# Performance work log

Hardware: AMD Instinct MI355X
Metric: run time of the kernel (lower is better)

The kernel has to match this reference:

```python
import jax, jax.numpy as jnp
import numpy as np

H = 1.0  # primo_h
N_GRID = 768


def _grid_mesh(n):
    ii, jj = np.meshgrid(np.arange(n - 1), np.arange(n - 1), indexing='ij')
    v00 = (ii * n + jj).ravel(); v10 = ((ii + 1) * n + jj).ravel()
    v01 = (ii * n + jj + 1).ravel(); v11 = ((ii + 1) * n + jj + 1).ravel()
    tri1 = np.stack([v00, v10, v01], 1); tri2 = np.stack([v10, v11, v01], 1)
    return np.concatenate([tri1, tri2], 0).astype(np.int32)  # [F,3]


def _face_adjacency(faces):
    # faces: [F,3] -> edges [E,2] (sorted vertex pairs), face_ids [E,2]
    F = faces.shape[0]
    fe = np.stack([faces[:, [0, 1]], faces[:, [1, 2]], faces[:, [2, 0]]], 1).reshape(-1, 2)
    fe = np.sort(fe, axis=1)
    fid = np.repeat(np.arange(F, dtype=np.int32), 3)
    order = np.lexsort((fe[:, 1], fe[:, 0]))
    fs, fi = fe[order], fid[order]
    same = np.all(fs[:-1] == fs[1:], axis=1)
    k = np.nonzero(same)[0]
    edges = fs[k].astype(np.int32)
    face_ids = np.stack([fi[k], fi[k + 1]], 1).astype(np.int32)
    return edges, face_ids


def setup_inputs() -> dict:
    key = jax.random.key(0)
    k1, k2, k3 = jax.random.split(key, 3)
    faces_np = _grid_mesh(N_GRID)                      # [F,3]
    edges_np, face_ids_np = _face_adjacency(faces_np)  # [E,2],[E,2]
    F = faces_np.shape[0]
    V = N_GRID * N_GRID
    return {
        'transformed_prism': jax.random.normal(k1, (F, 3, 3), dtype=jnp.float32),
        'rotations': jax.random.normal(k2, (F, 3, 3), dtype=jnp.float32),
        'verts': jax.random.normal(k3, (1, V, 3), dtype=jnp.float32),
        'faces': jnp.asarray(faces_np.T),       # [3,F], matches torch forward arg
        'edges': jnp.asarray(edges_np),
        'face_ids': jnp.asarray(face_ids_np),
    }


def _verts_id_face(Ft, E, Q):
    # Ft: [F,3] faces; E: [e,2] edge vertex ids; Q: [e,2] adjacent face ids
    fa, fb = Ft[Q[:, 0]], Ft[Q[:, 1]]  # [e,3]

    def find(fv, tgt):
        return jnp.where(fv[:, 0] == tgt, 0,
               jnp.where(fv[:, 1] == tgt, 1,
               jnp.where(fv[:, 2] == tgt, 2, -1)))

    return jnp.stack([find(fa, E[:, 0]), find(fa, E[:, 1]),
                      find(fb, E[:, 0]), find(fb, E[:, 1])], axis=1)  # [e,4]


def reference(transformed_prism, rotations, verts, faces, edges, face_ids):
    tp = transformed_prism
    bs = verts.shape[0]
    v = verts.reshape(-1, 3)
    Ft = faces.T  # [F,3]

    # per-face normals (vectorized version of the original per-face loop)
    e1 = tp[:, 0] - tp[:, 1]
    e2 = tp[:, 0] - tp[:, 2]
    nrm = jnp.cross(e1, e2)
    normals = nrm / jnp.linalg.norm(nrm, axis=-1, keepdims=True)  # [F,3]

    # face areas
    p1, p2, p3 = v[Ft[:, 0]], v[Ft[:, 1]], v[Ft[:, 2]]
    face_areas = 0.5 * jnp.linalg.norm(jnp.cross(p2 - p1, p3 - p1), axis=1)

    # faithful to original: normals indexed by edge VERTEX ids
    n1, n2 = normals[edges[:, 0]], normals[edges[:, 1]]
    fid1, fid2 = face_ids[:, 0], face_ids[:, 1]
    r1, r2 = rotations[fid1], rotations[fid2]

    ftv = _verts_id_face(Ft, edges, face_ids)  # [e,4]
    v1_p1, v2_p1 = tp[fid1, ftv[:, 0]], tp[fid1, ftv[:, 1]]
    v1_p2, v2_p2 = tp[fid2, ftv[:, 2]], tp[fid2, ftv[:, 3]]

    p1n1 = jnp.einsum('ec,ecd->ed', n1, r1)
    p1n2 = jnp.einsum('ec,ecd->ed', n2, r1)
    p2n1 = jnp.einsum('ec,ecd->ed', n1, r2)
    p2n2 = jnp.einsum('ec,ecd->ed', n2, r2)

    A = jnp.stack([v1_p1 + p1n1 * H, v2_p1 + p1n2 * H,
                   v1_p1 - p1n1 * H, v2_p1 - p1n2 * H], axis=1)  # [e,4,3]
    B = jnp.stack([v1_p2 + p2n1 * H, v2_p2 + p2n2 * H,
                   v1_p2 - p2n1 * H, v2_p2 - p2n2 * H], axis=1)
    D = A - B

    # coeff[p,q] = 2^{-|i_p-i_q|-|j_p-j_q|}, (i,j) over {0,1}^2
    idx = jnp.array([[0, 0], [0, 1], [1, 0], [1, 1]], dtype=jnp.float32)
    coeff = 2.0 ** (-jnp.abs(idx[:, None] - idx[None, :]).sum(-1))  # [4,4]
    pair = jnp.einsum('epc,eqc->epq', D, D)
    energy = (pair * coeff).sum((1, 2)) / 9.0  # [e]

    weight = jnp.sum((v[edges[:, 0]] - v[edges[:, 1]]) ** 2, axis=1) \
             / (face_areas[fid1] + face_areas[fid2])
    return (energy * weight).sum() / bs
```

## Files before the change

### kernel.cpp

```cpp
#include <hip/hip_runtime.h>


#define BI 8
#define BJ 32
#define T2ROW 288
#define VROW  100
#define NSTRIDE 99
#define T2_CH 648
#define V_CH  250
#define NORM_CNT 297
#define HALO_CNT 192

struct __attribute__((aligned(4))) F4s { float a, b, c, d; };
struct F3 { float x, y, z; };
struct R9 { float v[9]; };

__device__ __forceinline__ R9 load9(const float* __restrict__ p) {
    R9 r;
    F4s u0 = *(const F4s*)p;
    F4s u1 = *(const F4s*)(p + 4);
    r.v[0] = u0.a; r.v[1] = u0.b; r.v[2] = u0.c; r.v[3] = u0.d;
    r.v[4] = u1.a; r.v[5] = u1.b; r.v[6] = u1.c; r.v[7] = u1.d;
    r.v[8] = p[8];
    return r;
}

__device__ __forceinline__ int imin(int a, int b) { return a < b ? a : b; }
__device__ __forceinline__ int imax(int a, int b) { return a > b ? a : b; }

__device__ __forceinline__ void gload_lds16(const float* gp, float* lp) {
    __builtin_amdgcn_global_load_lds(
        (const __attribute__((address_space(1))) void*)gp,
        (__attribute__((address_space(3))) void*)lp, 16, 0, 0);
}

__device__ __forceinline__ F3 normal_of(const R9& r) {
    float e1x = r.v[0] - r.v[3], e1y = r.v[1] - r.v[4], e1z = r.v[2] - r.v[5];
    float e2x = r.v[0] - r.v[6], e2y = r.v[1] - r.v[7], e2z = r.v[2] - r.v[8];
    float nx = e1y * e2z - e1z * e2y;
    float ny = e1z * e2x - e1x * e2z;
    float nz = e1x * e2y - e1y * e2x;
    float inv = 1.0f / sqrtf(nx * nx + ny * ny + nz * nz);
    F3 o; o.x = nx * inv; o.y = ny * inv; o.z = nz * inv; return o;
}

__device__ __forceinline__ float tri_area_p(const float* p, const float* q,
                                            const float* r) {
    float ax = q[0] - p[0], ay = q[1] - p[1], az = q[2] - p[2];
    float bx = r[0] - p[0], by = r[1] - p[1], bz = r[2] - p[2];
    float cx = ay * bz - az * by, cy = az * bx - ax * bz, cz = ax * by - ay * bx;
    return 0.5f * sqrtf(cx * cx + cy * cy + cz * cz);
}

__device__ __forceinline__ float edge_ew(const float* u1, const float* u2,
                                         const float* w1, const float* w2,
                                         const float* rA, const float* rB,
                                         const F3& n1, const F3& n2,
                                         const float* pa, const float* pb,
                                         float asum) {
    float ux = u1[0] - u2[0], uy = u1[1] - u2[1], uz = u1[2] - u2[2];
    float wx = w1[0] - w2[0], wy = w1[1] - w2[1], wz = w1[2] - w2[2];

    float d0 = rA[0] - rB[0], d1 = rA[1] - rB[1], d2 = rA[2] - rB[2];
    float d3 = rA[3] - rB[3], d4 = rA[4] - rB[4], d5 = rA[5] - rB[5];
    float d6 = rA[6] - rB[6], d7 = rA[7] - rB[7], d8 = rA[8] - rB[8];

    float ax = n1.x * d0 + n1.y * d3 + n1.z * d6;
    float ay = n1.x * d1 + n1.y * d4 + n1.z * d7;
    float az = n1.x * d2 + n1.y * d5 + n1.z * d8;
    float bx = n2.x * d0 + n2.y * d3 + n2.z * d6;
    float by = n2.x * d1 + n2.y * d4 + n2.z * d7;
    float bz = n2.x * d2 + n2.y * d5 + n2.z * d8;

    float uu = ux * ux + uy * uy + uz * uz;
    float ww = wx * wx + wy * wy + wz * wz;
    float uw = ux * wx + uy * wy + uz * wz;
    float aa = ax * ax + ay * ay + az * az;
    float bb = bx * bx + by * by + bz * bz;
    float ab = ax * bx + ay * by + az * bz;
    float energy = (3.0f * (uu + ww + uw) + (aa + bb + ab)) * (1.0f / 9.0f);

    float dx = pa[0] - pb[0], dy = pa[1] - pb[1], dz = pa[2] - pb[2];
    return energy * (dx * dx + dy * dy + dz * dz) / asum;
}

__global__ __launch_bounds__(256) void fused_kernel(
        const float* __restrict__ tp,
        const float* __restrict__ rot,
        const float* __restrict__ verts,
        double* __restrict__ partials,
        int n) {
    const int m = n - 1;
    const int Q = m * m;
    const int F = 2 * Q;
    const int V = n * n;
    const int tid = threadIdx.x;
    const int i0 = blockIdx.y * BI;
    const int j0 = blockIdx.x * BJ;
    const int w = tid >> 5;
    const int l = tid & 31;
    const int i = i0 + w;
    const int j = j0 + l;
    const int wv = tid >> 6;
    const int lane = tid & 63;

    __shared__ __attribute__((aligned(16))) float sT2m[9 * T2ROW];
    __shared__ __attribute__((aligned(16))) float sR2m[9 * T2ROW];
    __shared__ __attribute__((aligned(16))) float sVm[10 * VROW];
    __shared__ float sN[9 * NSTRIDE];
    __shared__ float sT2h[9 * 12];
    __shared__ float sR2h[9 * 12];
    __shared__ float sVh[10 * 4];
    __shared__ double sred[4];

    int f1 = imin(i, m - 1) * m + imin(j, m - 1);
    R9 t1 = load9(tp  + (size_t)9 * f1);
    R9 r1 = load9(rot + (size_t)9 * f1);

#pragma unroll
    for (int it = 0; it < 7; ++it) {
        int ws = it * 4 + wv;
        if (ws < 22) {
            int a = ws >= 11;
            int wl = a ? ws - 11 : ws;
            int chunk = wl * 64 + lane;
            if (chunk < T2_CH) {
                int r = chunk / 72, c = chunk - r * 72;
                int gi = imin(i0 - 1 + r, m - 1);
                int g = 9 * (Q + gi * m + j0) + 4 * c;
                g = imin(g, 9 * F - 4);
                gload_lds16((a ? rot : tp) + g,
                            (a ? sR2m : sT2m) + chunk * 4);
            }
        } else if (ws < 26) {
            int chunk = (ws - 22) * 64 + lane;
            if (chunk < V_CH) {
                int r = chunk / 25, c = chunk - r * 25;
                int vr = imax(imin(i0 - 1 + r, n - 1), 0);
                int g = 3 * (vr * n + j0) + 4 * c;
                g = imin(g, 3 * V - 4);
                gload_lds16(verts + g, sVm + chunk * 4);
            }
        }
    }

    float hval = 0.0f;
    float* hdst = nullptr;
    if (tid < HALO_CNT) {
        if (tid < 162) {
            int a = tid >= 81;
            int t = a ? tid - 81 : tid;
            int r = t / 9, k = t - 9 * r;
            int gi = imin(i0 - 1 + r, m - 1);
            int face = Q + gi * m + (j0 - 1);
            hval = (a ? rot : tp)[9 * face + k];
            hdst = (a ? sR2h : sT2h) + r * 12 + k;
        } else {
            int t = tid - 162;
            int r = t / 3, k = t - 3 * r;
            int vr = imax(imin(i0 - 1 + r, n - 1), 0);
            int g = imax(3 * (vr * n + (j0 - 1)) + k, 0);
            hval = verts[g];
            hdst = sVh + r * 4 + k;
        }
    }

    R9 nraw[2];
    int nofs[2];
#pragma unroll
    for (int it = 0; it < 2; ++it) {
        int s = tid + 256 * it;
        bool act = s < NORM_CNT;
        int sc = act ? s : 0;
        int r = sc / 33, c = sc - 33 * r;
        int gi = imin(i0 + r, n - 1);
        int gj = imin(j0 + c, n - 1);
        nraw[it] = load9(tp + (size_t)9 * (gi * n + gj));
        nofs[it] = act ? (r * NSTRIDE + 3 * c) : -1;
    }

    if (hdst) *hdst = hval;
#pragma unroll
    for (int it = 0; it < 2; ++it) {
        if (nofs[it] >= 0) {
            F3 nm = normal_of(nraw[it]);
            sN[nofs[it]] = nm.x; sN[nofs[it] + 1] = nm.y; sN[nofs[it] + 2] = nm.z;
        }
    }

    __syncthreads();

    double term = 0.0;
    if (i < m && j < m) {
        const float* t2c = sT2m + (w + 1) * T2ROW + 9 * l;
        const float* r2c = sR2m + (w + 1) * T2ROW + 9 * l;
        const float* th  = sT2m + w * T2ROW + 9 * l;
        const float* rh  = sR2m + w * T2ROW + 9 * l;
        const float* tv  = l ? sT2m + (w + 1) * T2ROW + 9 * (l - 1)
                             : sT2h + (w + 1) * 12;
        const float* rv  = l ? sR2m + (w + 1) * T2ROW + 9 * (l - 1)
                             : sR2h + (w + 1) * 12;

        const float* p00 = sVm + (w + 1) * VROW + 3 * l;
        const float* p01 = p00 + 3;
        const float* p10 = sVm + (w + 2) * VROW + 3 * l;
        const float* p11 = p10 + 3;
        const float* pup = sVm + w * VROW + 3 * (l + 1);
        const float* plf = l ? sVm + (w + 2) * VROW + 3 * (l - 1)
                             : sVh + (w + 2) * 4;

        const float* na = sN + w * NSTRIDE + 3 * l;
        const float* nb = na + 3;
        const float* nc = sN + (w + 1) * NSTRIDE + 3 * l;
        F3 nA = { na[0], na[1], na[2] };
        F3 nB = { nb[0], nb[1], nb[2] };
        F3 nC = { nc[0], nc[1], nc[2] };

        float a1   = tri_area_p(p00, p10, p01);
        float a2c  = tri_area_p(p10, p11, p01);
        float a2up = tri_area_p(p00, p01, pup);
        float a2lf = tri_area_p(plf, p10, p00);

        float sum = edge_ew(t1.v + 6, t2c + 6, t1.v + 3, t2c + 0, r1.v, r2c,
                            nB, nC, p01, p10, a1 + a2c);
        float eh = edge_ew(t1.v + 0, th + 0, t1.v + 6, th + 3, r1.v, rh,
                           nA, nB, p00, p01, a1 + a2up);
        float ev = edge_ew(t1.v + 0, tv + 6, t1.v + 3, tv + 3, r1.v, rv,
                           nA, nC, p00, p10, a1 + a2lf);
        sum += (i > 0 ? eh : 0.0f);
        sum += (j > 0 ? ev : 0.0f);
        term = (double)sum;
    }

#pragma unroll
    for (int off = 32; off > 0; off >>= 1) term += __shfl_down(term, off, 64);
    if (lane == 0) sred[wv] = term;
    __syncthreads();
    if (tid == 0)
        partials[blockIdx.y * gridDim.x + blockIdx.x] =
            sred[0] + sred[1] + sred[2] + sred[3];
}

__global__ __launch_bounds__(256) void finalize_kernel(
        const double* __restrict__ partials, int P, float* __restrict__ out) {
    double s = 0.0;
    for (int i = threadIdx.x; i < P; i += 256) s += partials[i];
#pragma unroll
    for (int off = 32; off > 0; off >>= 1) s += __shfl_down(s, off, 64);
    __shared__ double sred[4];
    int lane = threadIdx.x & 63, wid = threadIdx.x >> 6;
    if (lane == 0) sred[wid] = s;
    __syncthreads();
    if (threadIdx.x == 0) out[0] = (float)(sred[0] + sred[1] + sred[2] + sred[3]);
}

extern "C" void kernel_launch(void* const* d_in, const int* in_sizes, int n_in,
                              void* d_out, int out_size, void* d_ws, size_t ws_size,
                              hipStream_t stream) {
    const float* tp    = (const float*)d_in[0];
    const float* rot   = (const float*)d_in[1];
    const float* verts = (const float*)d_in[2];

    int V = in_sizes[2] / 3;
    int n = (int)(sqrtf((float)V) + 0.5f);
    int m = n - 1;

    double* partials = (double*)d_ws;
    float*  out      = (float*)d_out;

    dim3 grid((m + BJ - 1) / BJ, (m + BI - 1) / BI);
    int P = grid.x * grid.y;
    fused_kernel<<<grid, 256, 0, stream>>>(tp, rot, verts, partials, n);
    finalize_kernel<<<1, 256, 0, stream>>>(partials, P, out);
}
```

Before: 145.5 us.

## Shrink tile to 8x8 single-wavefront blocks and fold halo into main loads

Changes the tile from 8x32 faces with 256 threads to 8x8 faces with a single 64-lane wavefront per block. The left halo column of second-triangle data is now loaded as part of the main tile, so the separate halo buffers and left-edge special cases for tp/rot go away. The block reduction no longer needs shared memory or a barrier, since one wave writes its partial directly. The cost is a larger halo fraction, with more redundant global loads per face, four times as many blocks, and a larger partials array for the finalize kernel to sum serially.

```diff
diff --git a/kernel.cpp b/kernel.cpp
--- a/kernel.cpp
+++ b/kernel.cpp
@@ -2,14 +2,13 @@
 
 
 #define BI 8
-#define BJ 32
-#define T2ROW 288
-#define VROW  100
-#define NSTRIDE 99
-#define T2_CH 648
-#define V_CH  250
-#define NORM_CNT 297
-#define HALO_CNT 192
+#define BJ 8
+#define T2ROW 84
+#define VROW  28
+#define NSTRIDE 28
+#define T2_CH 189
+#define V_CH  70
+#define NORM_CNT 81
 
 struct __attribute__((aligned(4))) F4s { float a, b, c, d; };
 struct F3 { float x, y, z; };
@@ -84,7 +83,7 @@
     return energy * (dx * dx + dy * dy + dz * dz) / asum;
 }
 
-__global__ __launch_bounds__(256) void fused_kernel(
+__global__ __launch_bounds__(64) void fused_kernel(
         const float* __restrict__ tp,
         const float* __restrict__ rot,
         const float* __restrict__ verts,
@@ -94,85 +93,67 @@
     const int Q = m * m;
     const int F = 2 * Q;
     const int V = n * n;
-    const int tid = threadIdx.x;
+    const int lane = threadIdx.x;
     const int i0 = blockIdx.y * BI;
     const int j0 = blockIdx.x * BJ;
-    const int w = tid >> 5;
-    const int l = tid & 31;
+    const int w = lane >> 3;
+    const int l = lane & 7;
     const int i = i0 + w;
     const int j = j0 + l;
-    const int wv = tid >> 6;
-    const int lane = tid & 63;
-
-    __shared__ __attribute__((aligned(16))) float sT2m[9 * T2ROW];
-    __shared__ __attribute__((aligned(16))) float sR2m[9 * T2ROW];
-    __shared__ __attribute__((aligned(16))) float sVm[10 * VROW];
+
+    __shared__ __attribute__((aligned(16))) float sT2[9 * T2ROW];
+    __shared__ __attribute__((aligned(16))) float sR2[9 * T2ROW];
+    __shared__ __attribute__((aligned(16))) float sV[10 * VROW];
+    __shared__ float sVh[10 * 4];
     __shared__ float sN[9 * NSTRIDE];
-    __shared__ float sT2h[9 * 12];
-    __shared__ float sR2h[9 * 12];
-    __shared__ float sVh[10 * 4];
-    __shared__ double sred[4];
 
     int f1 = imin(i, m - 1) * m + imin(j, m - 1);
     R9 t1 = load9(tp  + (size_t)9 * f1);
     R9 r1 = load9(rot + (size_t)9 * f1);
 
 #pragma unroll
-    for (int it = 0; it < 7; ++it) {
-        int ws = it * 4 + wv;
-        if (ws < 22) {
-            int a = ws >= 11;
-            int wl = a ? ws - 11 : ws;
-            int chunk = wl * 64 + lane;
-            if (chunk < T2_CH) {
-                int r = chunk / 72, c = chunk - r * 72;
+    for (int it = 0; it < 8; ++it) {
+        if (it < 6) {
+            int a = it >= 3;
+            int ch = (a ? it - 3 : it) * 64 + lane;
+            if (ch < T2_CH) {
+                int r = ch / 21, c = ch - 21 * r;
                 int gi = imin(i0 - 1 + r, m - 1);
-                int g = 9 * (Q + gi * m + j0) + 4 * c;
+                int g = 9 * (Q + gi * m + (j0 - 1)) + 4 * c;
                 g = imin(g, 9 * F - 4);
                 gload_lds16((a ? rot : tp) + g,
-                            (a ? sR2m : sT2m) + chunk * 4);
+                            (a ? sR2 : sT2) + ch * 4);
             }
-        } else if (ws < 26) {
-            int chunk = (ws - 22) * 64 + lane;
-            if (chunk < V_CH) {
-                int r = chunk / 25, c = chunk - r * 25;
+        } else {
+            int ch = (it - 6) * 64 + lane;
+            if (ch < V_CH) {
+                int r = ch / 7, c = ch - 7 * r;
                 int vr = imax(imin(i0 - 1 + r, n - 1), 0);
                 int g = 3 * (vr * n + j0) + 4 * c;
                 g = imin(g, 3 * V - 4);
-                gload_lds16(verts + g, sVm + chunk * 4);
+                gload_lds16(verts + g, sV + ch * 4);
             }
         }
     }
 
     float hval = 0.0f;
     float* hdst = nullptr;
-    if (tid < HALO_CNT) {
-        if (tid < 162) {
-            int a = tid >= 81;
-            int t = a ? tid - 81 : tid;
-            int r = t / 9, k = t - 9 * r;
-            int gi = imin(i0 - 1 + r, m - 1);
-            int face = Q + gi * m + (j0 - 1);
-            hval = (a ? rot : tp)[9 * face + k];
-            hdst = (a ? sR2h : sT2h) + r * 12 + k;
-        } else {
-            int t = tid - 162;
-            int r = t / 3, k = t - 3 * r;
-            int vr = imax(imin(i0 - 1 + r, n - 1), 0);
-            int g = imax(3 * (vr * n + (j0 - 1)) + k, 0);
-            hval = verts[g];
-            hdst = sVh + r * 4 + k;
-        }
+    if (lane < 30) {
+        int r = lane / 3, k = lane - 3 * r;
+        int vr = imax(imin(i0 - 1 + r, n - 1), 0);
+        int g = imax(3 * (vr * n + (j0 - 1)) + k, 0);
+        hval = verts[g];
+        hdst = sVh + r * 4 + k;
     }
 
     R9 nraw[2];
     int nofs[2];
 #pragma unroll
     for (int it = 0; it < 2; ++it) {
-        int s = tid + 256 * it;
+        int s = lane + 64 * it;
         bool act = s < NORM_CNT;
         int sc = act ? s : 0;
-        int r = sc / 33, c = sc - 33 * r;
+        int r = sc / 9, c = sc - 9 * r;
         int gi = imin(i0 + r, n - 1);
         int gj = imin(j0 + c, n - 1);
         nraw[it] = load9(tp + (size_t)9 * (gi * n + gj));
@@ -192,21 +173,19 @@
 
     double term = 0.0;
     if (i < m && j < m) {
-        const float* t2c = sT2m + (w + 1) * T2ROW + 9 * l;
-        const float* r2c = sR2m + (w + 1) * T2ROW + 9 * l;
-        const float* th  = sT2m + w * T2ROW + 9 * l;
-        const float* rh  = sR2m + w * T2ROW + 9 * l;
-        const float* tv  = l ? sT2m + (w + 1) * T2ROW + 9 * (l - 1)
-                             : sT2h + (w + 1) * 12;
-        const float* rv  = l ? sR2m + (w + 1) * T2ROW + 9 * (l - 1)
-                             : sR2h + (w + 1) * 12;
-
-        const float* p00 = sVm + (w + 1) * VROW + 3 * l;
+        const float* t2c = sT2 + (w + 1) * T2ROW + 9 * (l + 1);
+        const float* r2c = sR2 + (w + 1) * T2ROW + 9 * (l + 1);
+        const float* th  = sT2 + w * T2ROW + 9 * (l + 1);
+        const float* rh  = sR2 + w * T2ROW + 9 * (l + 1);
+        const float* tv  = sT2 + (w + 1) * T2ROW + 9 * l;
+        const float* rv  = sR2 + (w + 1) * T2ROW + 9 * l;
+
+        const float* p00 = sV + (w + 1) * VROW + 3 * l;
         const float* p01 = p00 + 3;
-        const float* p10 = sVm + (w + 2) * VROW + 3 * l;
+        const float* p10 = sV + (w + 2) * VROW + 3 * l;
         const float* p11 = p10 + 3;
-        const float* pup = sVm + w * VROW + 3 * (l + 1);
-        const float* plf = l ? sVm + (w + 2) * VROW + 3 * (l - 1)
+        const float* pup = sV + w * VROW + 3 * (l + 1);
+        const float* plf = l ? sV + (w + 2) * VROW + 3 * (l - 1)
                              : sVh + (w + 2) * 4;
 
         const float* na = sN + w * NSTRIDE + 3 * l;
@@ -234,11 +213,8 @@
 
 #pragma unroll
     for (int off = 32; off > 0; off >>= 1) term += __shfl_down(term, off, 64);
-    if (lane == 0) sred[wv] = term;
-    __syncthreads();
-    if (tid == 0)
-        partials[blockIdx.y * gridDim.x + blockIdx.x] =
-            sred[0] + sred[1] + sred[2] + sred[3];
+    if (lane == 0)
+        partials[blockIdx.y * gridDim.x + blockIdx.x] = term;
 }
 
 __global__ __launch_bounds__(256) void finalize_kernel(
@@ -270,6 +246,6 @@
 
     dim3 grid((m + BJ - 1) / BJ, (m + BI - 1) / BI);
     int P = grid.x * grid.y;
-    fused_kernel<<<grid, 256, 0, stream>>>(tp, rot, verts, partials, n);
+    fused_kernel<<<grid, 64, 0, stream>>>(tp, rot, verts, partials, n);
     finalize_kernel<<<1, 256, 0, stream>>>(partials, P, out);
 }
```

Result: slower. 159.5 us (+9.6%).

## Make blocks persistent over several tiles with double-buffered LDS prefetch

Applied to the files above, without the earlier changes.

Each block now handles three consecutive 8x32 tiles and double-buffers the shared-memory staging, so the next tile's async global-to-LDS loads and register loads are issued before the current tile is computed. The separate left-halo face loads are folded into a wider main DMA row of 75 chunks. This aims to hide load latency behind compute and cut per-block startup cost. In exchange, LDS use roughly doubles, which may lower occupancy, and there are fewer blocks across the GPU.

```diff
diff --git a/kernel.cpp b/kernel.cpp
--- a/kernel.cpp
+++ b/kernel.cpp
@@ -1,19 +1,18 @@
 #include <hip/hip_runtime.h>
 
 
-#define BI 8
-#define BJ 32
-#define T2ROW 288
-#define VROW  100
-#define NSTRIDE 99
-#define T2_CH 648
-#define V_CH  250
-#define NORM_CNT 297
-#define HALO_CNT 192
+#define FST 300
+#define F_SLOTS 675
+#define VST 100
+#define V_SLOTS 250
+#define NST 99
+#define NCNT 297
+#define TPB 3
 
 struct __attribute__((aligned(4))) F4s { float a, b, c, d; };
 struct F3 { float x, y, z; };
 struct R9 { float v[9]; };
+struct TileRegs { R9 t1, r1, nraw0, nraw1; float hval; };
 
 __device__ __forceinline__ R9 load9(const float* __restrict__ p) {
     R9 r;
@@ -95,123 +94,122 @@
     const int F = 2 * Q;
     const int V = n * n;
     const int tid = threadIdx.x;
-    const int i0 = blockIdx.y * BI;
-    const int j0 = blockIdx.x * BJ;
+    const int wv = tid >> 6;
+    const int lane = tid & 63;
     const int w = tid >> 5;
     const int l = tid & 31;
-    const int i = i0 + w;
-    const int j = j0 + l;
-    const int wv = tid >> 6;
-    const int lane = tid & 63;
-
-    __shared__ __attribute__((aligned(16))) float sT2m[9 * T2ROW];
-    __shared__ __attribute__((aligned(16))) float sR2m[9 * T2ROW];
-    __shared__ __attribute__((aligned(16))) float sVm[10 * VROW];
-    __shared__ float sN[9 * NSTRIDE];
-    __shared__ float sT2h[9 * 12];
-    __shared__ float sR2h[9 * 12];
-    __shared__ float sVh[10 * 4];
+
+    const int nTj = (m + 31) / 32;
+    const int nTi = (m + 7) / 8;
+    const int nT = nTi * nTj;
+
+    __shared__ __attribute__((aligned(16))) float sT2[2][9 * FST];
+    __shared__ __attribute__((aligned(16))) float sR2[2][9 * FST];
+    __shared__ __attribute__((aligned(16))) float sV[2][10 * VST];
+    __shared__ float sN[2][9 * NST];
+    __shared__ float sVh[2][10 * 4];
     __shared__ double sred[4];
 
-    int f1 = imin(i, m - 1) * m + imin(j, m - 1);
-    R9 t1 = load9(tp  + (size_t)9 * f1);
-    R9 r1 = load9(rot + (size_t)9 * f1);
-
+    auto stage_dma = [&](int p, int i0, int j0) {
 #pragma unroll
-    for (int it = 0; it < 7; ++it) {
-        int ws = it * 4 + wv;
-        if (ws < 22) {
-            int a = ws >= 11;
-            int wl = a ? ws - 11 : ws;
-            int chunk = wl * 64 + lane;
-            if (chunk < T2_CH) {
-                int r = chunk / 72, c = chunk - r * 72;
-                int gi = imin(i0 - 1 + r, m - 1);
-                int g = 9 * (Q + gi * m + j0) + 4 * c;
-                g = imin(g, 9 * F - 4);
-                gload_lds16((a ? rot : tp) + g,
-                            (a ? sR2m : sT2m) + chunk * 4);
+        for (int it = 0; it < 7; ++it) {
+            int ws = it * 4 + wv;
+            if (ws < 22) {
+                int a = ws >= 11;
+                int wl = a ? ws - 11 : ws;
+                int ch = wl * 64 + lane;
+                if (ch < F_SLOTS) {
+                    int r = ch / 75, c = ch - 75 * r;
+                    int gi = imin(i0 - 1 + r, m - 1);
+                    int g = 9 * (Q + gi * m + (j0 - 1)) + 4 * c;
+                    g = imin(g, 9 * F - 4);
+                    gload_lds16((a ? rot : tp) + g,
+                                (a ? sR2[p] : sT2[p]) + ch * 4);
+                }
+            } else if (ws < 26) {
+                int ch = (ws - 22) * 64 + lane;
+                if (ch < V_SLOTS) {
+                    int r = ch / 25, c = ch - 25 * r;
+                    int vr = imax(imin(i0 - 1 + r, n - 1), 0);
+                    int g = 3 * (vr * n + j0) + 4 * c;
+                    g = imin(g, 3 * V - 4);
+                    gload_lds16(verts + g, sV[p] + ch * 4);
+                }
             }
-        } else if (ws < 26) {
-            int chunk = (ws - 22) * 64 + lane;
-            if (chunk < V_CH) {
-                int r = chunk / 25, c = chunk - r * 25;
-                int vr = imax(imin(i0 - 1 + r, n - 1), 0);
-                int g = 3 * (vr * n + j0) + 4 * c;
-                g = imin(g, 3 * V - 4);
-                gload_lds16(verts + g, sVm + chunk * 4);
-            }
-        }
-    }
-
-    float hval = 0.0f;
-    float* hdst = nullptr;
-    if (tid < HALO_CNT) {
-        if (tid < 162) {
-            int a = tid >= 81;
-            int t = a ? tid - 81 : tid;
-            int r = t / 9, k = t - 9 * r;
-            int gi = imin(i0 - 1 + r, m - 1);
-            int face = Q + gi * m + (j0 - 1);
-            hval = (a ? rot : tp)[9 * face + k];
-            hdst = (a ? sR2h : sT2h) + r * 12 + k;
-        } else {
-            int t = tid - 162;
-            int r = t / 3, k = t - 3 * r;
+        }
+    };
+
+    auto stage_regs = [&](TileRegs& tr, int i0, int j0) {
+        int i = i0 + w, j = j0 + l;
+        int f1 = imin(i, m - 1) * m + imin(j, m - 1);
+        tr.t1 = load9(tp  + (size_t)9 * f1);
+        tr.r1 = load9(rot + (size_t)9 * f1);
+        {
+            int s = tid;
+            int r = s / 33, c = s - 33 * r;
+            int gi = imin(i0 + r, n - 1), gj = imin(j0 + c, n - 1);
+            tr.nraw0 = load9(tp + (size_t)9 * (size_t)(gi * n + gj));
+        }
+        {
+            int s = tid + 256;
+            int sc = (s < NCNT) ? s : 0;
+            int r = sc / 33, c = sc - 33 * r;
+            int gi = imin(i0 + r, n - 1), gj = imin(j0 + c, n - 1);
+            tr.nraw1 = load9(tp + (size_t)9 * (size_t)(gi * n + gj));
+        }
+        tr.hval = 0.0f;
+        if (tid < 30) {
+            int r = tid / 3, k = tid - 3 * r;
             int vr = imax(imin(i0 - 1 + r, n - 1), 0);
-            int g = imax(3 * (vr * n + (j0 - 1)) + k, 0);
-            hval = verts[g];
-            hdst = sVh + r * 4 + k;
-        }
-    }
-
-    R9 nraw[2];
-    int nofs[2];
-#pragma unroll
-    for (int it = 0; it < 2; ++it) {
-        int s = tid + 256 * it;
-        bool act = s < NORM_CNT;
-        int sc = act ? s : 0;
-        int r = sc / 33, c = sc - 33 * r;
-        int gi = imin(i0 + r, n - 1);
-        int gj = imin(j0 + c, n - 1);
-        nraw[it] = load9(tp + (size_t)9 * (gi * n + gj));
-        nofs[it] = act ? (r * NSTRIDE + 3 * c) : -1;
-    }
-
-    if (hdst) *hdst = hval;
-#pragma unroll
-    for (int it = 0; it < 2; ++it) {
-        if (nofs[it] >= 0) {
-            F3 nm = normal_of(nraw[it]);
-            sN[nofs[it]] = nm.x; sN[nofs[it] + 1] = nm.y; sN[nofs[it] + 2] = nm.z;
-        }
-    }
-
-    __syncthreads();
-
-    double term = 0.0;
-    if (i < m && j < m) {
-        const float* t2c = sT2m + (w + 1) * T2ROW + 9 * l;
-        const float* r2c = sR2m + (w + 1) * T2ROW + 9 * l;
-        const float* th  = sT2m + w * T2ROW + 9 * l;
-        const float* rh  = sR2m + w * T2ROW + 9 * l;
-        const float* tv  = l ? sT2m + (w + 1) * T2ROW + 9 * (l - 1)
-                             : sT2h + (w + 1) * 12;
-        const float* rv  = l ? sR2m + (w + 1) * T2ROW + 9 * (l - 1)
-                             : sR2h + (w + 1) * 12;
-
-        const float* p00 = sVm + (w + 1) * VROW + 3 * l;
+            tr.hval = verts[imax(3 * (vr * n + (j0 - 1)) + k, 0)];
+        }
+    };
+
+    auto write_regs = [&](int p, TileRegs& tr) {
+        {
+            int s = tid;
+            int r = s / 33, c = s - 33 * r;
+            F3 nm = normal_of(tr.nraw0);
+            int o = r * NST + 3 * c;
+            sN[p][o] = nm.x; sN[p][o + 1] = nm.y; sN[p][o + 2] = nm.z;
+        }
+        if (tid + 256 < NCNT) {
+            int s = tid + 256;
+            int r = s / 33, c = s - 33 * r;
+            F3 nm = normal_of(tr.nraw1);
+            int o = r * NST + 3 * c;
+            sN[p][o] = nm.x; sN[p][o + 1] = nm.y; sN[p][o + 2] = nm.z;
+        }
+        if (tid < 30) {
+            int r = tid / 3, k = tid - 3 * r;
+            sVh[p][r * 4 + k] = tr.hval;
+        }
+    };
+
+    auto compute_tile = [&](int p, int i0, int j0, const TileRegs& tr) -> double {
+        int i = i0 + w, j = j0 + l;
+        if (i >= m || j >= m) return 0.0;
+        const float* fT = sT2[p];
+        const float* fR = sR2[p];
+        const float* t2c = fT + (w + 1) * FST + 9 * (l + 1);
+        const float* r2c = fR + (w + 1) * FST + 9 * (l + 1);
+        const float* th  = fT + w * FST + 9 * (l + 1);
+        const float* rh  = fR + w * FST + 9 * (l + 1);
+        const float* tv  = fT + (w + 1) * FST + 9 * l;
+        const float* rv  = fR + (w + 1) * FST + 9 * l;
+
+        const float* vb = sV[p];
+        const float* p00 = vb + (w + 1) * VST + 3 * l;
         const float* p01 = p00 + 3;
-        const float* p10 = sVm + (w + 2) * VROW + 3 * l;
+        const float* p10 = vb + (w + 2) * VST + 3 * l;
         const float* p11 = p10 + 3;
-        const float* pup = sVm + w * VROW + 3 * (l + 1);
-        const float* plf = l ? sVm + (w + 2) * VROW + 3 * (l - 1)
-                             : sVh + (w + 2) * 4;
-
-        const float* na = sN + w * NSTRIDE + 3 * l;
+        const float* pup = vb + w * VST + 3 * (l + 1);
+        const float* plf = l ? vb + (w + 2) * VST + 3 * (l - 1)
+                             : sVh[p] + (w + 2) * 4;
+
+        const float* na = sN[p] + w * NST + 3 * l;
         const float* nb = na + 3;
-        const float* nc = sN + (w + 1) * NSTRIDE + 3 * l;
+        const float* nc = sN[p] + (w + 1) * NST + 3 * l;
         F3 nA = { na[0], na[1], na[2] };
         F3 nB = { nb[0], nb[1], nb[2] };
         F3 nC = { nc[0], nc[1], nc[2] };
@@ -221,24 +219,69 @@
         float a2up = tri_area_p(p00, p01, pup);
         float a2lf = tri_area_p(plf, p10, p00);
 
-        float sum = edge_ew(t1.v + 6, t2c + 6, t1.v + 3, t2c + 0, r1.v, r2c,
-                            nB, nC, p01, p10, a1 + a2c);
-        float eh = edge_ew(t1.v + 0, th + 0, t1.v + 6, th + 3, r1.v, rh,
-                           nA, nB, p00, p01, a1 + a2up);
-        float ev = edge_ew(t1.v + 0, tv + 6, t1.v + 3, tv + 3, r1.v, rv,
-                           nA, nC, p00, p10, a1 + a2lf);
+        float sum = edge_ew(tr.t1.v + 6, t2c + 6, tr.t1.v + 3, t2c + 0,
+                            tr.r1.v, r2c, nB, nC, p01, p10, a1 + a2c);
+        float eh = edge_ew(tr.t1.v + 0, th + 0, tr.t1.v + 6, th + 3,
+                           tr.r1.v, rh, nA, nB, p00, p01, a1 + a2up);
+        float ev = edge_ew(tr.t1.v + 0, tv + 6, tr.t1.v + 3, tv + 3,
+                           tr.r1.v, rv, nA, nC, p00, p10, a1 + a2lf);
         sum += (i > 0 ? eh : 0.0f);
         sum += (j > 0 ? ev : 0.0f);
-        term = (double)sum;
+        return (double)sum;
+    };
+
+    const int tau0 = blockIdx.x * TPB;
+    TileRegs regA, regB;
+
+    {
+        int tau = tau0;
+        if (tau < nT) {
+            int ti = tau / nTj, tj = tau - ti * nTj;
+            int i0 = ti * 8, j0 = tj * 32;
+            stage_dma(0, i0, j0);
+            stage_regs(regA, i0, j0);
+            write_regs(0, regA);
+        }
     }
-
+    __syncthreads();
+
+    double wsum = 0.0;
 #pragma unroll
-    for (int off = 32; off > 0; off >>= 1) term += __shfl_down(term, off, 64);
-    if (lane == 0) sred[wv] = term;
+    for (int tt = 0; tt < TPB; ++tt) {
+        const int p = tt & 1;
+        const int tau = tau0 + tt;
+        const bool live = tau < nT;
+        int ti = tau / nTj, tj = tau - ti * nTj;
+        const int i0 = ti * 8, j0 = tj * 32;
+
+        const int taun = tau + 1;
+        const bool liven = (tt < TPB - 1) && (taun < nT);
+        int tin = taun / nTj, tjn = taun - tin * nTj;
+        const int i0n = tin * 8, j0n = tjn * 32;
+
+        if (liven) {
+            stage_dma(p ^ 1, i0n, j0n);
+            if (tt & 1) stage_regs(regA, i0n, j0n);
+            else        stage_regs(regB, i0n, j0n);
+        }
+        __builtin_amdgcn_sched_barrier(0);
+
+        if (live) wsum += compute_tile(p, i0, j0, (tt & 1) ? regB : regA);
+        __builtin_amdgcn_sched_barrier(0);
+
+        if (liven) {
+            if (tt & 1) write_regs(p ^ 1, regA);
+            else        write_regs(p ^ 1, regB);
+        }
+        if (tt < TPB - 1) __syncthreads();
+    }
+
+#pragma unroll
+    for (int off = 32; off > 0; off >>= 1) wsum += __shfl_down(wsum, off, 64);
+    if (lane == 0) sred[wv] = wsum;
     __syncthreads();
     if (tid == 0)
-        partials[blockIdx.y * gridDim.x + blockIdx.x] =
-            sred[0] + sred[1] + sred[2] + sred[3];
+        partials[blockIdx.x] = sred[0] + sred[1] + sred[2] + sred[3];
 }
 
 __global__ __launch_bounds__(256) void finalize_kernel(
@@ -268,8 +311,10 @@
     double* partials = (double*)d_ws;
     float*  out      = (float*)d_out;
 
-    dim3 grid((m + BJ - 1) / BJ, (m + BI - 1) / BI);
-    int P = grid.x * grid.y;
-    fused_kernel<<<grid, 256, 0, stream>>>(tp, rot, verts, partials, n);
-    finalize_kernel<<<1, 256, 0, stream>>>(partials, P, out);
-}
+    int nTj = (m + 31) / 32, nTi = (m + 7) / 8;
+    int nT = nTi * nTj;
+    int nBlocks = (nT + TPB - 1) / TPB;
+
+    fused_kernel<<<nBlocks, 256, 0, stream>>>(tp, rot, verts, partials, n);
+    finalize_kernel<<<1, 256, 0, stream>>>(partials, nBlocks, out);
+}
```

Result: slower. 151.4 us (+4.0%).

## Precompute per-vertex normals in a separate kernel and stage them via async LDS loads

Applied to the files above, without the earlier changes.

Adds a pre-pass kernel that computes a normal for each of the first V faces of tp and writes them compactly to workspace. The main kernel then loads a tile of these normals straight into shared memory with the same 16-byte global-to-LDS path used for the other tiles, so it no longer loads 9 floats per entry and computes normals itself, including the halo entries that neighbouring blocks recompute. The cost is an extra launch plus a write and re-read of the normal array, and the workspace now has to be large enough past a fixed offset.

```diff
diff --git a/kernel.cpp b/kernel.cpp
--- a/kernel.cpp
+++ b/kernel.cpp
@@ -5,11 +5,12 @@
 #define BJ 32
 #define T2ROW 288
 #define VROW  100
-#define NSTRIDE 99
+#define NROW  100
 #define T2_CH 648
 #define V_CH  250
-#define NORM_CNT 297
+#define N_CH  225
 #define HALO_CNT 192
+#define NRM_OFS 32768
 
 struct __attribute__((aligned(4))) F4s { float a, b, c, d; };
 struct F3 { float x, y, z; };
@@ -84,10 +85,22 @@
     return energy * (dx * dx + dy * dy + dz * dz) / asum;
 }
 
+__global__ __launch_bounds__(256) void normal_precompute(
+        const float* __restrict__ tp, float* __restrict__ nrm, int V) {
+    int v = blockIdx.x * 256 + threadIdx.x;
+    if (v < V) {
+        F3 nm = normal_of(load9(tp + (size_t)9 * v));
+        nrm[3 * v]     = nm.x;
+        nrm[3 * v + 1] = nm.y;
+        nrm[3 * v + 2] = nm.z;
+    }
+}
+
 __global__ __launch_bounds__(256) void fused_kernel(
         const float* __restrict__ tp,
         const float* __restrict__ rot,
         const float* __restrict__ verts,
+        const float* __restrict__ nrm,
         double* __restrict__ partials,
         int n) {
     const int m = n - 1;
@@ -107,7 +120,7 @@
     __shared__ __attribute__((aligned(16))) float sT2m[9 * T2ROW];
     __shared__ __attribute__((aligned(16))) float sR2m[9 * T2ROW];
     __shared__ __attribute__((aligned(16))) float sVm[10 * VROW];
-    __shared__ float sN[9 * NSTRIDE];
+    __shared__ __attribute__((aligned(16))) float sNm[9 * NROW];
     __shared__ float sT2h[9 * 12];
     __shared__ float sR2h[9 * 12];
     __shared__ float sVh[10 * 4];
@@ -118,7 +131,7 @@
     R9 r1 = load9(rot + (size_t)9 * f1);
 
 #pragma unroll
-    for (int it = 0; it < 7; ++it) {
+    for (int it = 0; it < 8; ++it) {
         int ws = it * 4 + wv;
         if (ws < 22) {
             int a = ws >= 11;
@@ -141,6 +154,15 @@
                 g = imin(g, 3 * V - 4);
                 gload_lds16(verts + g, sVm + chunk * 4);
             }
+        } else if (ws < 30) {
+            int chunk = (ws - 26) * 64 + lane;
+            if (chunk < N_CH) {
+                int r = chunk / 25, c = chunk - r * 25;
+                int gi = imin(i0 + r, n - 1);
+                int g = 3 * (gi * n + j0) + 4 * c;
+                g = imin(g, 3 * V - 4);
+                gload_lds16(nrm + g, sNm + chunk * 4);
+            }
         }
     }
 
@@ -164,29 +186,7 @@
             hdst = sVh + r * 4 + k;
         }
     }
-
-    R9 nraw[2];
-    int nofs[2];
-#pragma unroll
-    for (int it = 0; it < 2; ++it) {
-        int s = tid + 256 * it;
-        bool act = s < NORM_CNT;
-        int sc = act ? s : 0;
-        int r = sc / 33, c = sc - 33 * r;
-        int gi = imin(i0 + r, n - 1);
-        int gj = imin(j0 + c, n - 1);
-        nraw[it] = load9(tp + (size_t)9 * (gi * n + gj));
-        nofs[it] = act ? (r * NSTRIDE + 3 * c) : -1;
-    }
-
     if (hdst) *hdst = hval;
-#pragma unroll
-    for (int it = 0; it < 2; ++it) {
-        if (nofs[it] >= 0) {
-            F3 nm = normal_of(nraw[it]);
-            sN[nofs[it]] = nm.x; sN[nofs[it] + 1] = nm.y; sN[nofs[it] + 2] = nm.z;
-        }
-    }
 
     __syncthreads();
 
@@ -209,9 +209,9 @@
         const float* plf = l ? sVm + (w + 2) * VROW + 3 * (l - 1)
                              : sVh + (w + 2) * 4;
 
-        const float* na = sN + w * NSTRIDE + 3 * l;
+        const float* na = sNm + w * NROW + 3 * l;
         const float* nb = na + 3;
-        const float* nc = sN + (w + 1) * NSTRIDE + 3 * l;
+        const float* nc = sNm + (w + 1) * NROW + 3 * l;
         F3 nA = { na[0], na[1], na[2] };
         F3 nB = { nb[0], nb[1], nb[2] };
         F3 nC = { nc[0], nc[1], nc[2] };
@@ -266,10 +266,13 @@
     int m = n - 1;
 
     double* partials = (double*)d_ws;
+    float*  nrm      = (float*)((char*)d_ws + NRM_OFS);
     float*  out      = (float*)d_out;
+
+    normal_precompute<<<(V + 255) / 256, 256, 0, stream>>>(tp, nrm, V);
 
     dim3 grid((m + BJ - 1) / BJ, (m + BI - 1) / BI);
     int P = grid.x * grid.y;
-    fused_kernel<<<grid, 256, 0, stream>>>(tp, rot, verts, partials, n);
+    fused_kernel<<<grid, 256, 0, stream>>>(tp, rot, verts, nrm, partials, n);
     finalize_kernel<<<1, 256, 0, stream>>>(partials, P, out);
 }
```

Result: slower. 156.6 us (+7.6%).
